# Performance work log

Hardware: AMD Instinct MI355X
Metric: run time of the kernel (lower is better)

## Reference

```python
import jax, jax.numpy as jnp
import numpy as np

N, E, R = 100000, 600000, 128
_INNER = 2  # _inner_mlp_mult


def _mlp(x, W1, b1, W2, b2):
    # 2-layer MLP: Linear -> ReLU -> Linear
    return jnp.maximum(x @ W1 + b1, 0.0) @ W2 + b2


def setup_inputs() -> dict:
    key = jax.random.key(0)
    ks = jax.random.split(key, 12)
    def w(k, shape):
        return (jax.random.normal(k, shape, jnp.float32) / np.sqrt(shape[0])).astype(jnp.float32)
    H = R * _INNER  # hidden width = 256
    return {
        "node_rep": jax.random.normal(ks[0], (N, R), jnp.float32),
        "edge_attr": jax.random.normal(ks[1], (E, R), jnp.float32),
        "edge_src": jax.random.randint(ks[2], (E,), 0, N, jnp.int32),
        "edge_dst": jax.random.randint(ks[3], (E,), 0, N, jnp.int32),
        # edge_mlp_0: in 3R -> H -> R
        "W1e": w(ks[4], (3 * R, H)), "b1e": jnp.zeros((H,), jnp.float32),
        "W2e": w(ks[5], (H, R)),     "b2e": jnp.zeros((R,), jnp.float32),
        # node_mlp: in 2R -> H -> R
        "W1n": w(ks[6], (2 * R, H)), "b1n": jnp.zeros((H,), jnp.float32),
        "W2n": w(ks[7], (H, R)),     "b2n": jnp.zeros((R,), jnp.float32),
    }


def reference(node_rep, edge_attr, W1e, b1e, W2e, b2e, W1n, b1n, W2n, b2n,
              edge_src, edge_dst):
    n_nodes, rep_dim = node_rep.shape
    # gather_from_ptensors(node_rep, G, edge): per-edge gather of the two
    # endpoint node features -> [E, 2R]
    node2edge = jnp.concatenate([node_rep[edge_src], node_rep[edge_dst]], axis=-1)
    # edge update: MLP over [edge_attr | node2edge] -> [E, R]
    edge_out = _mlp(jnp.concatenate([edge_attr, node2edge], axis=-1),
                    W1e, b1e, W2e, b2e)
    # gather_from_ptensors(edge_out, G, node): scatter-add edge features to
    # both incident nodes -> [N, R]
    edge2node = jnp.zeros((n_nodes, rep_dim), edge_out.dtype)
    edge2node = edge2node.at[edge_src].add(edge_out).at[edge_dst].add(edge_out)
    # node update: MLP over [node_rep | edge2node] -> [N, R]
    node_out = _mlp(jnp.concatenate([node_rep, edge2node], axis=-1),
                    W1n, b1n, W2n, b2n)
    return (node_out, edge_out)
```

## Files before the change

kernel.cpp:

```cpp
#include <hip/hip_runtime.h>

typedef __attribute__((ext_vector_type(8))) short short8;
typedef __attribute__((ext_vector_type(4))) float f32x4;

#define NN 100000
#define NE 600000
#define RR 128
#define HH 256
#define NB_SCAN 98
#define SEGB 16384

typedef const __attribute__((address_space(1))) void* gvp;
typedef __attribute__((address_space(3))) void* lvp;
typedef __attribute__((address_space(3))) char* lcp;

__device__ __forceinline__ unsigned short f2bf(float f) {
    unsigned u = __builtin_bit_cast(unsigned, f);
    u = (u + 0x7fffu + ((u >> 16) & 1u)) >> 16;
    return (unsigned short)u;
}

__device__ __forceinline__ unsigned pkbf(float lo, float hi) {
    unsigned a = __builtin_bit_cast(unsigned, lo) + 0x8000u;
    unsigned b = __builtin_bit_cast(unsigned, hi) + 0x8000u;
    return __builtin_amdgcn_perm(b, a, 0x07060302);
}
__device__ __forceinline__ float bflo(unsigned u) {
    return __builtin_bit_cast(float, u << 16);
}
__device__ __forceinline__ float bfhi(unsigned u) {
    return __builtin_bit_cast(float, u & 0xffff0000u);
}

__device__ __forceinline__ int swz(int byteoff, int row) {
    return byteoff ^ ((row & 7) << 4);
}

__device__ __forceinline__ void packw(const float* __restrict__ src,
                                      unsigned short* __restrict__ dst,
                                      int KS, int C, int t) {
    int l = t & 63, ks = (t >> 6) % KS, tile = t / (64 * KS);
    int col = tile * 16 + (l & 15);
    int krow = ks * 32 + (l >> 4) * 8;
    uint4 u;
    u.x = pkbf(src[(krow + 0) * C + col], src[(krow + 1) * C + col]);
    u.y = pkbf(src[(krow + 2) * C + col], src[(krow + 3) * C + col]);
    u.z = pkbf(src[(krow + 4) * C + col], src[(krow + 5) * C + col]);
    u.w = pkbf(src[(krow + 6) * C + col], src[(krow + 7) * C + col]);
    *reinterpret_cast<uint4*>(dst + (size_t)t * 8) = u;
}

__global__ __launch_bounds__(256) void prep_kernel(
    const float* __restrict__ W1e, const float* __restrict__ W2e,
    const float* __restrict__ W1n, const float* __restrict__ W2n,
    const float* __restrict__ node_rep,
    unsigned short* __restrict__ w1ep, unsigned short* __restrict__ w2ep,
    unsigned short* __restrict__ w1np, unsigned short* __restrict__ w2np,
    unsigned short* __restrict__ nr16)
{
    const int b = blockIdx.x;
    if (b >= 112) {
        int i = (b - 112) * 256 + threadIdx.x;
        if (i < NN * RR / 4) {
            float4 v = *reinterpret_cast<const float4*>(node_rep + (size_t)i * 4);
            uint2 u;
            u.x = pkbf(v.x, v.y);
            u.y = pkbf(v.z, v.w);
            *reinterpret_cast<uint2*>(nr16 + (size_t)i * 4) = u;
        }
        return;
    }
    if (b < 48)      { packw(W1e, w1ep, 12, 256, b * 256 + threadIdx.x); }
    else if (b < 64) { packw(W2e, w2ep,  8, 128, (b - 48) * 256 + threadIdx.x); }
    else if (b < 96) { packw(W1n, w1np,  8, 256, (b - 64) * 256 + threadIdx.x); }
    else             { packw(W2n, w2np,  8, 128, (b - 96) * 256 + threadIdx.x); }
}

__global__ __launch_bounds__(256) void count_kernel(const int* __restrict__ esrc,
                                                    const int* __restrict__ edst,
                                                    int* __restrict__ cnt) {
    int i = blockIdx.x * 256 + threadIdx.x;
    if (i < NE) {
        atomicAdd(&cnt[esrc[i]], 1);
        atomicAdd(&cnt[edst[i]], 1);
    }
}

__global__ __launch_bounds__(1024) void scan_part(const int* __restrict__ cnt,
                                                  int* __restrict__ excl,
                                                  int* __restrict__ bsum) {
    __shared__ int wsum[16];
    const int tid = threadIdx.x;
    const int lane = tid & 63, w = tid >> 6;
    int i = blockIdx.x * 1024 + tid;
    int v = (i < NN) ? cnt[i] : 0;
    int s = v;
    #pragma unroll
    for (int d = 1; d < 64; d <<= 1) {
        int t = __shfl_up(s, d, 64);
        if (lane >= d) s += t;
    }
    if (lane == 63) wsum[w] = s;
    __syncthreads();
    if (w == 0) {
        int x = (lane < 16) ? wsum[lane] : 0;
        int sx = x;
        #pragma unroll
        for (int d = 1; d < 16; d <<= 1) {
            int t = __shfl_up(sx, d, 64);
            if (lane >= d) sx += t;
        }
        if (lane < 16) wsum[lane] = sx - x;
        if (lane == 15) bsum[blockIdx.x] = sx;
    }
    __syncthreads();
    if (i < NN) excl[i] = wsum[w] + (s - v);
}

__global__ void scan_tops(int* __restrict__ bsum, int* __restrict__ offs_nn) {
    if (threadIdx.x == 0) {
        int run = 0;
        for (int b = 0; b < NB_SCAN; ++b) { int t = bsum[b]; bsum[b] = run; run += t; }
        *offs_nn = run;
    }
}

__global__ __launch_bounds__(1024) void scan_add(int* __restrict__ offs,
                                                 const int* __restrict__ bsum,
                                                 int* __restrict__ cur) {
    int i = blockIdx.x * 1024 + threadIdx.x;
    if (i < NN) { int v = offs[i] + bsum[blockIdx.x]; offs[i] = v; cur[i] = v; }
}

__global__ __launch_bounds__(256) void fill_kernel(const int* __restrict__ esrc,
                                                   const int* __restrict__ edst,
                                                   int* __restrict__ cur,
                                                   int* __restrict__ adj) {
    int i = blockIdx.x * 256 + threadIdx.x;
    if (i < NE) {
        int p = atomicAdd(&cur[esrc[i]], 1);
        adj[p] = i;
        int q = atomicAdd(&cur[edst[i]], 1);
        adj[q] = i;
    }
}

__global__ __launch_bounds__(512, 5) void edge_kernel(
    const unsigned short* __restrict__ nr16, const float* __restrict__ edge_attr,
    const int* __restrict__ esrc, const int* __restrict__ edst,
    const unsigned short* __restrict__ w1p, const float* __restrict__ b1,
    const unsigned short* __restrict__ w2p, const float* __restrict__ b2,
    float* __restrict__ edge_out, unsigned short* __restrict__ eo16)
{
    __shared__ char Sbuf[3 * SEGB];
    lcp SbufL = (lcp)Sbuf;
    const int tid = threadIdx.x;
    const int e0 = blockIdx.x * 64;
    const int lane = tid & 63, wave = tid >> 6;
    const int l15 = lane & 15, l4 = lane >> 4;

    const int c4 = tid & 31;
    const int row_b = tid >> 5;

    float4 ga[4];
    #pragma unroll
    for (int j = 0; j < 4; ++j) {
        int row = row_b + j * 16;
        ga[j] = *reinterpret_cast<const float4*>(edge_attr + (size_t)(e0 + row) * RR + c4 * 4);
    }

    {
        int r0 = wave * 8 + (lane >> 4);
        int r1 = r0 + 4;
        int i0 = esrc[e0 + r0];
        int i1 = esrc[e0 + r1];
        int j0 = edst[e0 + r0];
        int j1 = edst[e0 + r1];
        const char* gs0 = (const char*)nr16 + (size_t)i0 * 256 + (((lane & 15) ^ (r0 & 7)) << 4);
        const char* gs1 = (const char*)nr16 + (size_t)i1 * 256 + (((lane & 15) ^ (r1 & 7)) << 4);
        const char* gd0 = (const char*)nr16 + (size_t)j0 * 256 + (((lane & 15) ^ (r0 & 7)) << 4);
        const char* gd1 = (const char*)nr16 + (size_t)j1 * 256 + (((lane & 15) ^ (r1 & 7)) << 4);
        __builtin_amdgcn_global_load_lds((gvp)gs0, (lvp)(SbufL + SEGB + wave * 2048), 16, 0, 0);
        __builtin_amdgcn_global_load_lds((gvp)gs1, (lvp)(SbufL + SEGB + wave * 2048 + 1024), 16, 0, 0);
        __builtin_amdgcn_global_load_lds((gvp)gd0, (lvp)(SbufL + 2 * SEGB + wave * 2048), 16, 0, 0);
        __builtin_amdgcn_global_load_lds((gvp)gd1, (lvp)(SbufL + 2 * SEGB + wave * 2048 + 1024), 16, 0, 0);
    }

    #pragma unroll
    for (int j = 0; j < 4; ++j) {
        int row = row_b + j * 16;
        uint2 u; u.x = pkbf(ga[j].x, ga[j].y); u.y = pkbf(ga[j].z, ga[j].w);
        *reinterpret_cast<uint2*>(&Sbuf[swz(row * 256 + c4 * 8, row)]) = u;
    }
    __syncthreads();

    f32x4 acc[2][4] = {};
    const unsigned short* w1base = w1p + ((size_t)(2 * wave) * 12 * 64 + lane) * 8;

#define GEMM1_SEG(SEGIDX, SBASE)                                                     \
    _Pragma("unroll")                                                                \
    for (int kk2 = 0; kk2 < 4; ++kk2) {                                              \
        const int koel = kk2 * 32 + l4 * 8;                                          \
        short8 bfr[4];                                                               \
        _Pragma("unroll")                                                            \
        for (int et = 0; et < 4; ++et) {                                             \
            int rw = et * 16 + l15;                                                  \
            bfr[et] = *reinterpret_cast<const short8*>(                              \
                &Sbuf[(SBASE) + swz(rw * 256 + koel * 2, rw)]);                      \
        }                                                                            \
        _Pragma("unroll")                                                            \
        for (int ht = 0; ht < 2; ++ht) {                                             \
            short8 afr = *reinterpret_cast<const short8*>(                           \
                w1base + (size_t)(ht * 12 + (SEGIDX) * 4 + kk2) * 64 * 8);           \
            _Pragma("unroll")                                                        \
            for (int et = 0; et < 4; ++et)                                           \
                acc[ht][et] = __builtin_amdgcn_mfma_f32_16x16x32_bf16(               \
                    afr, bfr[et], acc[ht][et], 0, 0, 0);                             \
        }                                                                            \
    }

    GEMM1_SEG(0, 0)
    GEMM1_SEG(1, SEGB)
    GEMM1_SEG(2, 2 * SEGB)
    __syncthreads();
#undef GEMM1_SEG

    const int hbase = wave * 32;
    #pragma unroll
    for (int ht = 0; ht < 2; ++ht) {
        const int h0 = hbase + ht * 16 + l4 * 4;
        float4 bb = *reinterpret_cast<const float4*>(b1 + h0);
        #pragma unroll
        for (int et = 0; et < 4; ++et) {
            int e = et * 16 + l15;
            float x0 = fmaxf(acc[ht][et][0] + bb.x, 0.f);
            float x1 = fmaxf(acc[ht][et][1] + bb.y, 0.f);
            float x2 = fmaxf(acc[ht][et][2] + bb.z, 0.f);
            float x3 = fmaxf(acc[ht][et][3] + bb.w, 0.f);
            uint2 u; u.x = pkbf(x0, x1); u.y = pkbf(x2, x3);
            *reinterpret_cast<uint2*>(&Sbuf[swz(e * 512 + h0 * 2, e)]) = u;
        }
    }
    __syncthreads();

    f32x4 acc2[4] = {};
    const unsigned short* w2base = w2p + ((size_t)(wave * 8) * 64 + lane) * 8;
    #pragma unroll
    for (int ks = 0; ks < 8; ++ks) {
        const int koel = ks * 32 + l4 * 8;
        short8 afr = *reinterpret_cast<const short8*>(w2base + (size_t)ks * 64 * 8);
        #pragma unroll
        for (int et = 0; et < 4; ++et) {
            int rw = et * 16 + l15;
            short8 bfr = *reinterpret_cast<const short8*>(&Sbuf[swz(rw * 512 + koel * 2, rw)]);
            acc2[et] = __builtin_amdgcn_mfma_f32_16x16x32_bf16(afr, bfr, acc2[et], 0, 0, 0);
        }
    }

    const int c0 = wave * 16 + l4 * 4;
    uint2 pk[4];
    {
        float4 bb2 = *reinterpret_cast<const float4*>(b2 + c0);
        #pragma unroll
        for (int et = 0; et < 4; ++et) {
            int e = et * 16 + l15;
            float4 v;
            v.x = acc2[et][0] + bb2.x;
            v.y = acc2[et][1] + bb2.y;
            v.z = acc2[et][2] + bb2.z;
            v.w = acc2[et][3] + bb2.w;
            *reinterpret_cast<float4*>(edge_out + (size_t)(e0 + e) * RR + c0) = v;
            pk[et].x = pkbf(v.x, v.y);
            pk[et].y = pkbf(v.z, v.w);
        }
    }
    __syncthreads();

    #pragma unroll
    for (int et = 0; et < 4; ++et) {
        int e = et * 16 + l15;
        *reinterpret_cast<uint2*>(&Sbuf[swz(e * 256 + c0 * 2, e)]) = pk[et];
    }
    __syncthreads();

    {
        char* tile = (char*)eo16 + (size_t)blockIdx.x * 16384;
        #pragma unroll
        for (int it = 0; it < 2; ++it) {
            uint4 v = *reinterpret_cast<const uint4*>(&Sbuf[it * 8192 + tid * 16]);
            *reinterpret_cast<uint4*>(tile + it * 8192 + tid * 16) = v;
        }
    }
}

__global__ __launch_bounds__(512, 5) void node_kernel(
    const unsigned short* __restrict__ nr16,
    const int* __restrict__ offs, const int* __restrict__ adj,
    const unsigned short* __restrict__ eo16,
    const unsigned short* __restrict__ w1p, const float* __restrict__ b1,
    const unsigned short* __restrict__ w2p, const float* __restrict__ b2,
    float* __restrict__ out)
{
    __shared__ char Abuf[64 * 512];
    const int tid = threadIdx.x;
    const int n0 = blockIdx.x * 64;
    const int r = tid >> 3, t8 = tid & 7;
    const int n = n0 + r;
    const int nc = (n < NN) ? n : NN - 1;
    const char* eob = (const char*)eo16;

    {
        const uint4* src = reinterpret_cast<const uint4*>(nr16 + (size_t)nc * RR + t8 * 16);
        uint4 v0 = src[0], v1 = src[1];
        int b = r * 512 + t8 * 32;
        *reinterpret_cast<uint2*>(&Abuf[swz(b, r)])      = uint2{v0.x, v0.y};
        *reinterpret_cast<uint2*>(&Abuf[swz(b + 8, r)])  = uint2{v0.z, v0.w};
        *reinterpret_cast<uint2*>(&Abuf[swz(b + 16, r)]) = uint2{v1.x, v1.y};
        *reinterpret_cast<uint2*>(&Abuf[swz(b + 24, r)]) = uint2{v1.z, v1.w};
    }
    {
        f32x4 a0 = {}, a1 = {}, a2 = {}, a3 = {};
        const int sbase = t8 * 32;
        if (n < NN) {
            int p = offs[n];
            const int pe = offs[n + 1];
            for (; p + 1 < pe; p += 2) {
                int ea = adj[p], eb = adj[p + 1];
                int sa = sbase ^ ((ea & 7) << 4);
                int sb = sbase ^ ((eb & 7) << 4);
                uint4 xa = *reinterpret_cast<const uint4*>(eob + (size_t)ea * 256 + sa);
                uint4 ya = *reinterpret_cast<const uint4*>(eob + (size_t)ea * 256 + (sa ^ 16));
                uint4 xb = *reinterpret_cast<const uint4*>(eob + (size_t)eb * 256 + sb);
                uint4 yb = *reinterpret_cast<const uint4*>(eob + (size_t)eb * 256 + (sb ^ 16));
                a0[0] += bflo(xa.x); a0[1] += bfhi(xa.x); a0[2] += bflo(xa.y); a0[3] += bfhi(xa.y);
                a1[0] += bflo(xa.z); a1[1] += bfhi(xa.z); a1[2] += bflo(xa.w); a1[3] += bfhi(xa.w);
                a2[0] += bflo(ya.x); a2[1] += bfhi(ya.x); a2[2] += bflo(ya.y); a2[3] += bfhi(ya.y);
                a3[0] += bflo(ya.z); a3[1] += bfhi(ya.z); a3[2] += bflo(ya.w); a3[3] += bfhi(ya.w);
                a0[0] += bflo(xb.x); a0[1] += bfhi(xb.x); a0[2] += bflo(xb.y); a0[3] += bfhi(xb.y);
                a1[0] += bflo(xb.z); a1[1] += bfhi(xb.z); a1[2] += bflo(xb.w); a1[3] += bfhi(xb.w);
                a2[0] += bflo(yb.x); a2[1] += bfhi(yb.x); a2[2] += bflo(yb.y); a2[3] += bfhi(yb.y);
                a3[0] += bflo(yb.z); a3[1] += bfhi(yb.z); a3[2] += bflo(yb.w); a3[3] += bfhi(yb.w);
            }
            if (p < pe) {
                int e = adj[p];
                int sa = sbase ^ ((e & 7) << 4);
                uint4 xa = *reinterpret_cast<const uint4*>(eob + (size_t)e * 256 + sa);
                uint4 ya = *reinterpret_cast<const uint4*>(eob + (size_t)e * 256 + (sa ^ 16));
                a0[0] += bflo(xa.x); a0[1] += bfhi(xa.x); a0[2] += bflo(xa.y); a0[3] += bfhi(xa.y);
                a1[0] += bflo(xa.z); a1[1] += bfhi(xa.z); a1[2] += bflo(xa.w); a1[3] += bfhi(xa.w);
                a2[0] += bflo(ya.x); a2[1] += bfhi(ya.x); a2[2] += bflo(ya.y); a2[3] += bfhi(ya.y);
                a3[0] += bflo(ya.z); a3[1] += bfhi(ya.z); a3[2] += bflo(ya.w); a3[3] += bfhi(ya.w);
            }
        }
        uint2 u;
        int b = r * 512 + 256 + t8 * 32;
        u.x = pkbf(a0[0], a0[1]); u.y = pkbf(a0[2], a0[3]);
        *reinterpret_cast<uint2*>(&Abuf[swz(b, r)]) = u;
        u.x = pkbf(a1[0], a1[1]); u.y = pkbf(a1[2], a1[3]);
        *reinterpret_cast<uint2*>(&Abuf[swz(b + 8, r)]) = u;
        u.x = pkbf(a2[0], a2[1]); u.y = pkbf(a2[2], a2[3]);
        *reinterpret_cast<uint2*>(&Abuf[swz(b + 16, r)]) = u;
        u.x = pkbf(a3[0], a3[1]); u.y = pkbf(a3[2], a3[3]);
        *reinterpret_cast<uint2*>(&Abuf[swz(b + 24, r)]) = u;
    }
    __syncthreads();

    const int lane = tid & 63, wave = tid >> 6;
    const int l15 = lane & 15, l4 = lane >> 4;

    f32x4 accu[8] = {};
    const unsigned short* w1base = w1p + ((size_t)(2 * wave) * 8 * 64 + lane) * 8;
    #pragma unroll
    for (int kk = 0; kk < 8; ++kk) {
        const int koel = kk * 32 + l4 * 8;
        short8 bfr[4];
        #pragma unroll
        for (int et = 0; et < 4; ++et) {
            int rw = et * 16 + l15;
            bfr[et] = *reinterpret_cast<const short8*>(&Abuf[swz(rw * 512 + koel * 2, rw)]);
        }
        #pragma unroll
        for (int ht = 0; ht < 2; ++ht) {
            short8 afr = *reinterpret_cast<const short8*>(
                w1base + (size_t)(ht * 8 + kk) * 64 * 8);
            #pragma unroll
            for (int et = 0; et < 4; ++et)
                accu[ht * 4 + et] = __builtin_amdgcn_mfma_f32_16x16x32_bf16(afr, bfr[et], accu[ht * 4 + et], 0, 0, 0);
        }
    }
    __syncthreads();

    const int hbase = wave * 32;
    #pragma unroll
    for (int ht = 0; ht < 2; ++ht) {
        const int h0 = hbase + ht * 16 + l4 * 4;
        float4 bb = *reinterpret_cast<const float4*>(b1 + h0);
        #pragma unroll
        for (int et = 0; et < 4; ++et) {
            int e = et * 16 + l15;
            float x0 = fmaxf(accu[ht * 4 + et][0] + bb.x, 0.f);
            float x1 = fmaxf(accu[ht * 4 + et][1] + bb.y, 0.f);
            float x2 = fmaxf(accu[ht * 4 + et][2] + bb.z, 0.f);
            float x3 = fmaxf(accu[ht * 4 + et][3] + bb.w, 0.f);
            uint2 u; u.x = pkbf(x0, x1); u.y = pkbf(x2, x3);
            *reinterpret_cast<uint2*>(&Abuf[swz(e * 512 + h0 * 2, e)]) = u;
        }
    }
    __syncthreads();

    #pragma unroll
    for (int et = 0; et < 4; ++et) accu[et] = f32x4{0.f, 0.f, 0.f, 0.f};

    const unsigned short* w2base = w2p + ((size_t)(wave * 8) * 64 + lane) * 8;
    #pragma unroll
    for (int ks = 0; ks < 8; ++ks) {
        const int koel = ks * 32 + l4 * 8;
        short8 afr = *reinterpret_cast<const short8*>(w2base + (size_t)ks * 64 * 8);
        #pragma unroll
        for (int et = 0; et < 4; ++et) {
            int rw = et * 16 + l15;
            short8 bfr = *reinterpret_cast<const short8*>(&Abuf[swz(rw * 512 + koel * 2, rw)]);
            accu[et] = __builtin_amdgcn_mfma_f32_16x16x32_bf16(afr, bfr, accu[et], 0, 0, 0);
        }
    }

    {
        const int c0 = wave * 16 + l4 * 4;
        float4 bb = *reinterpret_cast<const float4*>(b2 + c0);
        #pragma unroll
        for (int et = 0; et < 4; ++et) {
            int nn2 = n0 + et * 16 + l15;
            if (nn2 < NN) {
                float4 v;
                v.x = accu[et][0] + bb.x;
                v.y = accu[et][1] + bb.y;
                v.z = accu[et][2] + bb.z;
                v.w = accu[et][3] + bb.w;
                *reinterpret_cast<float4*>(out + (size_t)nn2 * RR + c0) = v;
            }
        }
    }
}

extern "C" void kernel_launch(void* const* d_in, const int* in_sizes, int n_in,
                              void* d_out, int out_size, void* d_ws, size_t ws_size,
                              hipStream_t stream) {
    const float* node_rep  = (const float*)d_in[0];
    const float* edge_attr = (const float*)d_in[1];
    const int*   esrc      = (const int*)d_in[2];
    const int*   edst      = (const int*)d_in[3];
    const float* W1e = (const float*)d_in[4];
    const float* b1e = (const float*)d_in[5];
    const float* W2e = (const float*)d_in[6];
    const float* b2e = (const float*)d_in[7];
    const float* W1n = (const float*)d_in[8];
    const float* b1n = (const float*)d_in[9];
    const float* W2n = (const float*)d_in[10];
    const float* b2n = (const float*)d_in[11];

    float* out      = (float*)d_out;
    float* node_out = out;
    float* edge_out = out + (size_t)NN * RR;

    char* ws = (char*)d_ws;
    unsigned short* w1ep = (unsigned short*)ws;
    unsigned short* w2ep = w1ep + 98304;
    unsigned short* w1np = w2ep + 32768;
    unsigned short* w2np = w1np + 65536;
    size_t off = 458752;
    unsigned short* nr16 = (unsigned short*)(ws + off); off += (size_t)NN * RR * 2;
    unsigned short* eo16 = (unsigned short*)(ws + off); off += (size_t)NE * RR * 2;
    int* cnt  = (int*)(ws + off);               off += 400000;
    int* offs = (int*)(ws + off);               off += 400008;
    int* adj  = (int*)(ws + off);               off += 4800000;
    int* bsum = (int*)(ws + off);               off += 512;

    hipMemsetAsync(cnt, 0, (size_t)NN * sizeof(int), stream);

    prep_kernel<<<12612, 256, 0, stream>>>(W1e, W2e, W1n, W2n, node_rep,
                                           w1ep, w2ep, w1np, w2np, nr16);

    count_kernel<<<(NE + 255) / 256, 256, 0, stream>>>(esrc, edst, cnt);
    scan_part<<<NB_SCAN, 1024, 0, stream>>>(cnt, offs, bsum);
    scan_tops<<<1, 64, 0, stream>>>(bsum, offs + NN);
    scan_add<<<NB_SCAN, 1024, 0, stream>>>(offs, bsum, cnt);
    fill_kernel<<<(NE + 255) / 256, 256, 0, stream>>>(esrc, edst, cnt, adj);

    edge_kernel<<<NE / 64, 512, 0, stream>>>(nr16, edge_attr, esrc, edst,
                                             w1ep, b1e, w2ep, b2e, edge_out, eo16);

    node_kernel<<<(NN + 63) / 64, 512, 0, stream>>>(nr16, offs, adj, eo16,
                                                    w1np, b1n, w2np, b2n, node_out);
}
```

Baseline: 582.6 us.

## Pre-cast edge_attr to bf16 and DMA it into LDS in edge kernel

Adds a separate pass that converts edge_attr to bf16 in workspace. The edge kernel then loads it with global_load_lds async copies, alongside the node gathers, instead of doing register loads plus conversion. The edge kernel also stages fp32 edge_out through LDS for coalesced row stores and raises occupancy hints. This adds an extra full read/write pass over edge_attr and depends on enough workspace being available.

```diff
diff --git a/kernel.cpp b/kernel.cpp
--- a/kernel.cpp
+++ b/kernel.cpp
@@ -76,6 +76,18 @@
     else             { packw(W2n, w2np,  8, 128, (b - 96) * 256 + threadIdx.x); }
 }
 
+__global__ __launch_bounds__(256) void ea_cast(const float* __restrict__ src,
+                                               unsigned short* __restrict__ dst) {
+    size_t i = (size_t)blockIdx.x * 256 + threadIdx.x;
+    if (i < (size_t)NE * RR / 4) {
+        float4 v = *reinterpret_cast<const float4*>(src + i * 4);
+        uint2 u;
+        u.x = pkbf(v.x, v.y);
+        u.y = pkbf(v.z, v.w);
+        *reinterpret_cast<uint2*>(dst + i * 4) = u;
+    }
+}
+
 __global__ __launch_bounds__(256) void count_kernel(const int* __restrict__ esrc,
                                                     const int* __restrict__ edst,
                                                     int* __restrict__ cnt) {
@@ -145,7 +157,147 @@
     }
 }
 
-__global__ __launch_bounds__(512, 5) void edge_kernel(
+__global__ __launch_bounds__(512, 6) void edge_kernel_dma(
+    const unsigned short* __restrict__ nr16, const unsigned short* __restrict__ ea16,
+    const int* __restrict__ esrc, const int* __restrict__ edst,
+    const unsigned short* __restrict__ w1p, const float* __restrict__ b1,
+    const unsigned short* __restrict__ w2p, const float* __restrict__ b2,
+    float* __restrict__ edge_out, unsigned short* __restrict__ eo16)
+{
+    __shared__ char Sbuf[3 * SEGB];
+    lcp SbufL = (lcp)Sbuf;
+    const int tid = threadIdx.x;
+    const int e0 = blockIdx.x * 64;
+    const int lane = tid & 63, wave = tid >> 6;
+    const int l15 = lane & 15, l4 = lane >> 4;
+
+    {
+        int r0 = wave * 8 + (lane >> 4);
+        int r1 = r0 + 4;
+        int sw0 = ((lane & 15) ^ (r0 & 7)) << 4;
+        int sw1 = ((lane & 15) ^ (r1 & 7)) << 4;
+        const char* ga0 = (const char*)ea16 + (size_t)(e0 + r0) * 256 + sw0;
+        const char* ga1 = (const char*)ea16 + (size_t)(e0 + r1) * 256 + sw1;
+        __builtin_amdgcn_global_load_lds((gvp)ga0, (lvp)(SbufL + wave * 2048), 16, 0, 0);
+        __builtin_amdgcn_global_load_lds((gvp)ga1, (lvp)(SbufL + wave * 2048 + 1024), 16, 0, 0);
+        int i0 = esrc[e0 + r0];
+        int i1 = esrc[e0 + r1];
+        const char* gs0 = (const char*)nr16 + (size_t)i0 * 256 + sw0;
+        const char* gs1 = (const char*)nr16 + (size_t)i1 * 256 + sw1;
+        __builtin_amdgcn_global_load_lds((gvp)gs0, (lvp)(SbufL + SEGB + wave * 2048), 16, 0, 0);
+        __builtin_amdgcn_global_load_lds((gvp)gs1, (lvp)(SbufL + SEGB + wave * 2048 + 1024), 16, 0, 0);
+        int j0 = edst[e0 + r0];
+        int j1 = edst[e0 + r1];
+        const char* gd0 = (const char*)nr16 + (size_t)j0 * 256 + sw0;
+        const char* gd1 = (const char*)nr16 + (size_t)j1 * 256 + sw1;
+        __builtin_amdgcn_global_load_lds((gvp)gd0, (lvp)(SbufL + 2 * SEGB + wave * 2048), 16, 0, 0);
+        __builtin_amdgcn_global_load_lds((gvp)gd1, (lvp)(SbufL + 2 * SEGB + wave * 2048 + 1024), 16, 0, 0);
+    }
+    __syncthreads();
+
+    f32x4 accu[8] = {};
+    const unsigned short* w1base = w1p + ((size_t)(2 * wave) * 12 * 64 + lane) * 8;
+
+#define GEMM1_SEG(SEGIDX, SBASE)                                                     \
+    _Pragma("unroll")                                                                \
+    for (int kk2 = 0; kk2 < 4; ++kk2) {                                              \
+        const int koel = kk2 * 32 + l4 * 8;                                          \
+        short8 bfr[4];                                                               \
+        _Pragma("unroll")                                                            \
+        for (int et = 0; et < 4; ++et) {                                             \
+            int rw = et * 16 + l15;                                                  \
+            bfr[et] = *reinterpret_cast<const short8*>(                              \
+                &Sbuf[(SBASE) + swz(rw * 256 + koel * 2, rw)]);                      \
+        }                                                                            \
+        _Pragma("unroll")                                                            \
+        for (int ht = 0; ht < 2; ++ht) {                                             \
+            short8 afr = *reinterpret_cast<const short8*>(                           \
+                w1base + (size_t)(ht * 12 + (SEGIDX) * 4 + kk2) * 64 * 8);           \
+            _Pragma("unroll")                                                        \
+            for (int et = 0; et < 4; ++et)                                           \
+                accu[ht * 4 + et] = __builtin_amdgcn_mfma_f32_16x16x32_bf16(         \
+                    afr, bfr[et], accu[ht * 4 + et], 0, 0, 0);                       \
+        }                                                                            \
+    }
+
+    GEMM1_SEG(0, 0)
+    GEMM1_SEG(1, SEGB)
+    GEMM1_SEG(2, 2 * SEGB)
+    __syncthreads();
+#undef GEMM1_SEG
+
+    const int hbase = wave * 32;
+    #pragma unroll
+    for (int ht = 0; ht < 2; ++ht) {
+        const int h0 = hbase + ht * 16 + l4 * 4;
+        float4 bb = *reinterpret_cast<const float4*>(b1 + h0);
+        #pragma unroll
+        for (int et = 0; et < 4; ++et) {
+            int e = et * 16 + l15;
+            float x0 = fmaxf(accu[ht * 4 + et][0] + bb.x, 0.f);
+            float x1 = fmaxf(accu[ht * 4 + et][1] + bb.y, 0.f);
+            float x2 = fmaxf(accu[ht * 4 + et][2] + bb.z, 0.f);
+            float x3 = fmaxf(accu[ht * 4 + et][3] + bb.w, 0.f);
+            uint2 u; u.x = pkbf(x0, x1); u.y = pkbf(x2, x3);
+            *reinterpret_cast<uint2*>(&Sbuf[swz(e * 512 + h0 * 2, e)]) = u;
+        }
+    }
+    __syncthreads();
+
+    #pragma unroll
+    for (int et = 0; et < 4; ++et) accu[et] = f32x4{0.f, 0.f, 0.f, 0.f};
+
+    const unsigned short* w2base = w2p + ((size_t)(wave * 8) * 64 + lane) * 8;
+    #pragma unroll
+    for (int ks = 0; ks < 8; ++ks) {
+        const int koel = ks * 32 + l4 * 8;
+        short8 afr = *reinterpret_cast<const short8*>(w2base + (size_t)ks * 64 * 8);
+        #pragma unroll
+        for (int et = 0; et < 4; ++et) {
+            int rw = et * 16 + l15;
+            short8 bfr = *reinterpret_cast<const short8*>(&Sbuf[swz(rw * 512 + koel * 2, rw)]);
+            accu[et] = __builtin_amdgcn_mfma_f32_16x16x32_bf16(afr, bfr, accu[et], 0, 0, 0);
+        }
+    }
+    __syncthreads();
+
+    {
+        const int c0 = wave * 16 + l4 * 4;
+        float4 bb2 = *reinterpret_cast<const float4*>(b2 + c0);
+        #pragma unroll
+        for (int et = 0; et < 4; ++et) {
+            int e = et * 16 + l15;
+            float4 v;
+            v.x = accu[et][0] + bb2.x;
+            v.y = accu[et][1] + bb2.y;
+            v.z = accu[et][2] + bb2.z;
+            v.w = accu[et][3] + bb2.w;
+            *reinterpret_cast<float4*>(&Sbuf[swz(e * 512 + c0 * 4, e)]) = v;
+            uint2 u; u.x = pkbf(v.x, v.y); u.y = pkbf(v.z, v.w);
+            *reinterpret_cast<uint2*>(&Sbuf[2 * SEGB + swz(e * 256 + c0 * 2, e)]) = u;
+        }
+    }
+    __syncthreads();
+
+    {
+        char* ot = (char*)edge_out + (size_t)blockIdx.x * 32768;
+        #pragma unroll
+        for (int it = 0; it < 4; ++it) {
+            int idx = it * 8192 + tid * 16;
+            int row = idx >> 9, off = idx & 511;
+            uint4 v = *reinterpret_cast<const uint4*>(&Sbuf[row * 512 + (off ^ ((row & 7) << 4))]);
+            *reinterpret_cast<uint4*>(ot + idx) = v;
+        }
+        char* mt = (char*)eo16 + (size_t)blockIdx.x * 16384;
+        #pragma unroll
+        for (int it = 0; it < 2; ++it) {
+            uint4 v = *reinterpret_cast<const uint4*>(&Sbuf[2 * SEGB + it * 8192 + tid * 16]);
+            *reinterpret_cast<uint4*>(mt + it * 8192 + tid * 16) = v;
+        }
+    }
+}
+
+__global__ __launch_bounds__(512, 5) void edge_kernel_ga(
     const unsigned short* __restrict__ nr16, const float* __restrict__ edge_attr,
     const int* __restrict__ esrc, const int* __restrict__ edst,
     const unsigned short* __restrict__ w1p, const float* __restrict__ b1,
@@ -158,7 +310,6 @@
     const int e0 = blockIdx.x * 64;
     const int lane = tid & 63, wave = tid >> 6;
     const int l15 = lane & 15, l4 = lane >> 4;
-
     const int c4 = tid & 31;
     const int row_b = tid >> 5;
 
@@ -168,7 +319,6 @@
         int row = row_b + j * 16;
         ga[j] = *reinterpret_cast<const float4*>(edge_attr + (size_t)(e0 + row) * RR + c4 * 4);
     }
-
     {
         int r0 = wave * 8 + (lane >> 4);
         int r1 = r0 + 4;
@@ -185,7 +335,6 @@
         __builtin_amdgcn_global_load_lds((gvp)gd0, (lvp)(SbufL + 2 * SEGB + wave * 2048), 16, 0, 0);
         __builtin_amdgcn_global_load_lds((gvp)gd1, (lvp)(SbufL + 2 * SEGB + wave * 2048 + 1024), 16, 0, 0);
     }
-
     #pragma unroll
     for (int j = 0; j < 4; ++j) {
         int row = row_b + j * 16;
@@ -275,14 +424,12 @@
         }
     }
     __syncthreads();
-
     #pragma unroll
     for (int et = 0; et < 4; ++et) {
         int e = et * 16 + l15;
         *reinterpret_cast<uint2*>(&Sbuf[swz(e * 256 + c0 * 2, e)]) = pk[et];
     }
     __syncthreads();
-
     {
         char* tile = (char*)eo16 + (size_t)blockIdx.x * 16384;
         #pragma unroll
@@ -474,11 +621,16 @@
     int* offs = (int*)(ws + off);               off += 400008;
     int* adj  = (int*)(ws + off);               off += 4800000;
     int* bsum = (int*)(ws + off);               off += 512;
+    unsigned short* ea16 = (unsigned short*)(ws + off);
+    const size_t need = off + (size_t)NE * RR * 2;
+    const bool big = ws_size >= need;
 
     hipMemsetAsync(cnt, 0, (size_t)NN * sizeof(int), stream);
 
     prep_kernel<<<12612, 256, 0, stream>>>(W1e, W2e, W1n, W2n, node_rep,
                                            w1ep, w2ep, w1np, w2np, nr16);
+    if (big)
+        ea_cast<<<(NE * RR / 4 + 255) / 256, 256, 0, stream>>>(edge_attr, ea16);
 
     count_kernel<<<(NE + 255) / 256, 256, 0, stream>>>(esrc, edst, cnt);
     scan_part<<<NB_SCAN, 1024, 0, stream>>>(cnt, offs, bsum);
@@ -486,8 +638,12 @@
     scan_add<<<NB_SCAN, 1024, 0, stream>>>(offs, bsum, cnt);
     fill_kernel<<<(NE + 255) / 256, 256, 0, stream>>>(esrc, edst, cnt, adj);
 
-    edge_kernel<<<NE / 64, 512, 0, stream>>>(nr16, edge_attr, esrc, edst,
-                                             w1ep, b1e, w2ep, b2e, edge_out, eo16);
+    if (big)
+        edge_kernel_dma<<<NE / 64, 512, 0, stream>>>(nr16, ea16, esrc, edst,
+                                                     w1ep, b1e, w2ep, b2e, edge_out, eo16);
+    else
+        edge_kernel_ga<<<NE / 64, 512, 0, stream>>>(nr16, edge_attr, esrc, edst,
+                                                    w1ep, b1e, w2ep, b2e, edge_out, eo16);
 
     node_kernel<<<(NN + 63) / 64, 512, 0, stream>>>(nr16, offs, adj, eo16,
                                                     w1np, b1n, w2np, b2n, node_out);
```

After: 687.4 us. +18.0%, slower.
